# Performance work log

Measured on AMD Instinct MI355X. Metric: run time of the kernel, lower is better.

Reference implementation:

```python
import jax, jax.numpy as jnp
import numpy as np
import math

B, S, HID, L, NH, V, M = 8, 512, 768, 12, 12, 30522, 512
FF = 4 * HID
D = HID // NH


def sinusoidal_pe(seq_len, dim):
    pos = np.arange(seq_len, dtype=np.float32)[:, None]
    i = np.arange(dim // 2, dtype=np.float32)[None, :]
    ang = pos / np.power(10000.0, 2.0 * i / dim)
    pe = np.zeros((seq_len, dim), np.float32)
    pe[:, 0::2] = np.sin(ang)
    pe[:, 1::2] = np.cos(ang)
    return jnp.asarray(pe)


def setup_inputs() -> dict:
    key = jax.random.key(0)
    ks = iter(jax.random.split(key, 32))
    g = lambda sh: jax.random.normal(next(ks), sh, jnp.float32) * 0.02
    return {
        "token_ids": jax.random.randint(next(ks), (B, S), 0, V),
        "segment_info": jax.random.randint(next(ks), (B, S), 0, 2),
        "tok_emb": g((V, HID)),
        "seg_emb": g((3, HID)),
        "Wq": g((L, HID, HID)), "bq": jnp.zeros((L, HID)),
        "Wk": g((L, HID, HID)), "bk": jnp.zeros((L, HID)),
        "Wv": g((L, HID, HID)), "bv": jnp.zeros((L, HID)),
        "Wo": g((L, HID, HID)), "bo": jnp.zeros((L, HID)),
        "Wpk": g((L, HID, HID)),
        "Wpq": g((L, HID, HID)),
        "rel_emb": g((L, 2 * M, HID)),
        "ln1_g": jnp.ones((L, HID)), "ln1_b": jnp.zeros((L, HID)),
        "ln2_g": jnp.ones((L, HID)), "ln2_b": jnp.zeros((L, HID)),
        "W1": g((L, HID, FF)), "b1": jnp.zeros((L, FF)),
        "W2": g((L, FF, HID)), "b2": jnp.zeros((L, HID)),
        "lnf_g": jnp.ones((HID,)), "lnf_b": jnp.zeros((HID,)),
    }


def _ln(x, g, b):
    mu = x.mean(-1, keepdims=True)
    var = ((x - mu) ** 2).mean(-1, keepdims=True)
    return (x - mu) * jax.lax.rsqrt(var + 1e-5) * g + b


def _forward(token_ids, segment_info, tok_emb, seg_emb, layer_params, lnf_g, lnf_b):
    mask = token_ids != 0  # [B,S] valid-key mask
    x = tok_emb[token_ids] + sinusoidal_pe(S, HID)[None] + seg_emb[segment_info]
    qidx = jnp.arange(S)[:, None]
    # relative position bucket: clamp(q-k, -M, M-1) + M  -> [0, 2M)
    rel = jnp.clip(qidx - jnp.arange(S)[None, :], -M, M - 1) + M  # [S,S]
    scale = 1.0 / math.sqrt(3.0 * D)  # DeBERTa scales by sqrt(3d) for 3 score terms

    def body(x, p):
        (Wq, bq, Wk, bk, Wv, bv, Wo, bo, Wpk, Wpq, rel_e,
         l1g, l1b, l2g, l2b, W1, b1, W2, b2) = p
        # pre-norm attention sublayer
        h = _ln(x, l1g, l1b)
        q = (h @ Wq + bq).reshape(B, S, NH, D)
        k = (h @ Wk + bk).reshape(B, S, NH, D)
        v = (h @ Wv + bv).reshape(B, S, NH, D)
        c2c = jnp.einsum('bqhd,bkhd->bhqk', q, k)
        pk = (rel_e @ Wpk).reshape(2 * M, NH, D)
        pq = (rel_e @ Wpq).reshape(2 * M, NH, D)
        # content-to-position: Q_q . posK[rel(q,k)]
        c2p = jnp.einsum('bqhd,rhd->bhqr', q, pk)[:, :, qidx, rel]  # [B,NH,S,S]
        # position-to-content: K_k . posQ[rel(k,q)] -> gather over k rows then transpose
        p2c = jnp.einsum('bkhd,rhd->bhkr', k, pq)[:, :, qidx, rel]  # [B,NH,k,q]
        scores = (c2c + c2p + jnp.swapaxes(p2c, -1, -2)) * scale
        scores = jnp.where(mask[:, None, None, :], scores, -1e9)
        attn = jax.nn.softmax(scores, axis=-1)
        ctx = jnp.einsum('bhqk,bkhd->bqhd', attn, v).reshape(B, S, HID)
        x = x + ctx @ Wo + bo
        # pre-norm feedforward sublayer
        h2 = _ln(x, l2g, l2b)
        x = x + jax.nn.gelu(h2 @ W1 + b1, approximate=False) @ W2 + b2
        return x, None

    x, _ = jax.lax.scan(body, x, layer_params)
    return _ln(x, lnf_g, lnf_b)


def reference(token_ids, segment_info, tok_emb, seg_emb, Wq, bq, Wk, bk, Wv, bv,
              Wo, bo, Wpk, Wpq, rel_emb, ln1_g, ln1_b, ln2_g, ln2_b,
              W1, b1, W2, b2, lnf_g, lnf_b):
    lp = (Wq, bq, Wk, bk, Wv, bv, Wo, bo, Wpk, Wpq, rel_emb,
          ln1_g, ln1_b, ln2_g, ln2_b, W1, b1, W2, b2)
    return _forward(token_ids, segment_info, tok_emb, seg_emb, lp, lnf_g, lnf_b)
```

## Files before the change

### kernel.cpp

```cpp
#include <hip/hip_runtime.h>
#include <hip/hip_bf16.h>
#include <cstddef>
#include <cstdint>


constexpr int B   = 8;
constexpr int S   = 512;
constexpr int HID = 768;
constexpr int L   = 12;
constexpr int NH  = 12;
constexpr int D   = 64;
constexpr int FF  = 3072;
constexpr int M2  = 1024;
constexpr int NTOK = B * S;

using f32x4 = __attribute__((ext_vector_type(4))) float;
using s16x8 = __attribute__((ext_vector_type(8))) short;

__device__ inline float wave_sum(float v) {
#pragma unroll
  for (int o = 32; o > 0; o >>= 1) v += __shfl_xor(v, o, 64);
  return v;
}
__device__ inline unsigned short f2bf(float f) {
  __hip_bfloat16 h = __float2bfloat16(f);
  return *reinterpret_cast<unsigned short*>(&h);
}
__device__ inline float bf2f(unsigned short u) {
  union { unsigned int i; float f; } x;
  x.i = ((unsigned int)u) << 16;
  return x.f;
}
#define GLOAD16(gp, lp)                                                  \
  __builtin_amdgcn_global_load_lds(                                     \
      (const __attribute__((address_space(1))) void*)(gp),              \
      (__attribute__((address_space(3))) void*)(lp), 16, 0, 0)

__global__ void embed_kernel(const int* __restrict__ tok,
                             const int* __restrict__ seg,
                             const float* __restrict__ tok_emb,
                             const float* __restrict__ seg_emb,
                             float* __restrict__ x) {
  int row = blockIdx.x;
  int s = row & (S - 1);
  int t = tok[row];
  int sg = seg[row];
  for (int c = threadIdx.x; c < HID; c += blockDim.x) {
    int i = c >> 1;
    float ang = (float)s * powf(10000.0f, -2.0f * (float)i / (float)HID);
    float pe = (c & 1) ? cosf(ang) : sinf(ang);
    x[(size_t)row * HID + c] = tok_emb[(size_t)t * HID + c] + pe
                             + seg_emb[(size_t)sg * HID + c];
  }
}

template <int BF16OUT>
__global__ __launch_bounds__(256)
void ln_kernel(const float* __restrict__ in, void* __restrict__ outp,
               const float* __restrict__ g, const float* __restrict__ b,
               int nrows) {
  int wave = threadIdx.x >> 6, lane = threadIdx.x & 63;
  int row = blockIdx.x * 4 + wave;
  if (row >= nrows) return;
  const float* xr = in + (size_t)row * HID;
  float v[12];
  float s = 0.f;
#pragma unroll
  for (int i = 0; i < 12; i++) { v[i] = xr[lane + i * 64]; s += v[i]; }
  s = wave_sum(s);
  float mu = s * (1.0f / HID);
  float ss = 0.f;
#pragma unroll
  for (int i = 0; i < 12; i++) { float d = v[i] - mu; ss += d * d; }
  ss = wave_sum(ss);
  float inv = rsqrtf(ss * (1.0f / HID) + 1e-5f);
#pragma unroll
  for (int i = 0; i < 12; i++) {
    int c = lane + i * 64;
    float o = (v[i] - mu) * inv * g[c] + b[c];
    if (BF16OUT)
      ((unsigned short*)outp)[(size_t)row * HID + c] = f2bf(o);
    else
      ((float*)outp)[(size_t)row * HID + c] = o;
  }
}

__global__ __launch_bounds__(256)
void transpose6_kernel(const float* s0, const float* s1, const float* s2,
                       const float* s3, const float* s4, const float* s5,
                       unsigned short* __restrict__ dst) {
  const float* srcs[6] = {s0, s1, s2, s3, s4, s5};
  const float* src = srcs[blockIdx.z];
  unsigned short* d = dst + (size_t)blockIdx.z * HID * HID;
  __shared__ float tile[32][33];
  int nt = blockIdx.x * 32, kt = blockIdx.y * 32;
  int tx = threadIdx.x & 31, ty = threadIdx.x >> 5;
#pragma unroll
  for (int i = 0; i < 4; i++)
    tile[ty + i * 8][tx] = src[(size_t)(kt + ty + i * 8) * HID + nt + tx];
  __syncthreads();
#pragma unroll
  for (int i = 0; i < 4; i++)
    d[(size_t)(nt + ty + i * 8) * HID + kt + tx] = f2bf(tile[tx][ty + i * 8]);
}

__global__ __launch_bounds__(256)
void transpose_ff(const float* __restrict__ W1s, const float* __restrict__ W2s,
                  unsigned short* __restrict__ d1, unsigned short* __restrict__ d2) {
  const float* src = blockIdx.z ? W2s : W1s;
  unsigned short* dst = blockIdx.z ? d2 : d1;
  int K = blockIdx.z ? FF : HID;
  int N = blockIdx.z ? HID : FF;
  int nt, kt;
  if (blockIdx.z) { nt = blockIdx.y * 32; kt = blockIdx.x * 32; }
  else            { nt = blockIdx.x * 32; kt = blockIdx.y * 32; }
  __shared__ float tile[32][33];
  int tx = threadIdx.x & 31, ty = threadIdx.x >> 5;
#pragma unroll
  for (int i = 0; i < 4; i++)
    tile[ty + i * 8][tx] = src[(size_t)(kt + ty + i * 8) * N + nt + tx];
  __syncthreads();
#pragma unroll
  for (int i = 0; i < 4; i++)
    dst[(size_t)(nt + ty + i * 8) * K + kt + tx] = f2bf(tile[tx][ty + i * 8]);
}

__global__ void conv_bf16_kernel(const float* __restrict__ src,
                                 unsigned short* __restrict__ dst, int n) {
  int i = blockIdx.x * 256 + threadIdx.x;
  if (i < n) dst[i] = f2bf(src[i]);
}

__global__ void concat_bias(const float* __restrict__ bq,
                            const float* __restrict__ bk,
                            const float* __restrict__ bv,
                            float* __restrict__ bqkv) {
  int i = blockIdx.x * 256 + threadIdx.x;
  if (i >= L * 2304) return;
  int l = i / 2304, c = i % 2304;
  float v = (c < 768) ? bq[l * 768 + c]
          : (c < 1536) ? bk[l * 768 + c - 768] : bv[l * 768 + c - 1536];
  bqkv[i] = v;
}

template <int TN, int OUT_BF16, int GELU, int PARTIAL>
__global__ __launch_bounds__(256)
void mfma_gemm(const unsigned short* __restrict__ A,
               const unsigned short* __restrict__ Bt,
               const float* __restrict__ bias, const float* __restrict__ res,
               void* __restrict__ C, int Mr, int K, int N, int Kc) {
  constexpr int NW = TN / 32;
  __shared__ unsigned short As[128 * 32];
  __shared__ unsigned short Bs[TN * 32];
  int t = threadIdx.x, wave = t >> 6, lane = t & 63;
  int r0 = blockIdx.y * 128, n0 = blockIdx.x * TN;
  int kb = blockIdx.z * Kc;
  int wr = (wave >> 1) * 64;
  int wc = (wave & 1) * (TN / 2);

  f32x4 acc[4][NW] = {};
  int srow = lane >> 2, selem = (lane & 3) * 8;

  for (int k0 = kb; k0 < kb + Kc; k0 += 32) {
    __syncthreads();
    {
      const unsigned short* gA =
          A + (size_t)(r0 + wave * 32 + srow) * K + k0 + selem;
      unsigned short* lA = &As[(wave * 32) * 32];
      GLOAD16(gA, lA);
      GLOAD16(gA + (size_t)16 * K, lA + 16 * 32);
      if (TN == 128) {
        const unsigned short* gB =
            Bt + (size_t)(n0 + wave * 32 + srow) * K + k0 + selem;
        unsigned short* lB = &Bs[(wave * 32) * 32];
        GLOAD16(gB, lB);
        GLOAD16(gB + (size_t)16 * K, lB + 16 * 32);
      } else {
        const unsigned short* gB =
            Bt + (size_t)(n0 + wave * 16 + srow) * K + k0 + selem;
        GLOAD16(gB, &Bs[(wave * 16) * 32]);
      }
    }
    __syncthreads();

    s16x8 af[4], bf[NW];
#pragma unroll
    for (int m = 0; m < 4; m++)
      af[m] = *(const s16x8*)&As[(wr + m * 16 + (lane & 15)) * 32 + (lane >> 4) * 8];
#pragma unroll
    for (int n = 0; n < NW; n++)
      bf[n] = *(const s16x8*)&Bs[(wc + n * 16 + (lane & 15)) * 32 + (lane >> 4) * 8];
#pragma unroll
    for (int m = 0; m < 4; m++)
#pragma unroll
      for (int n = 0; n < NW; n++)
        acc[m][n] = __builtin_amdgcn_mfma_f32_16x16x32_bf16(af[m], bf[n],
                                                            acc[m][n], 0, 0, 0);
  }

  if (PARTIAL) {
    float* Cp = (float*)C + (size_t)blockIdx.z * Mr * N;
#pragma unroll
    for (int n = 0; n < NW; n++) {
      int c = n0 + wc + n * 16 + (lane & 15);
#pragma unroll
      for (int m = 0; m < 4; m++) {
        int rb = r0 + wr + m * 16 + ((lane >> 4) << 2);
#pragma unroll
        for (int j = 0; j < 4; j++)
          Cp[(size_t)(rb + j) * N + c] = acc[m][n][j];
      }
    }
    return;
  }
#pragma unroll
  for (int n = 0; n < NW; n++) {
    int c = n0 + wc + n * 16 + (lane & 15);
    float bv = bias ? bias[c] : 0.f;
#pragma unroll
    for (int m = 0; m < 4; m++) {
      int rb = r0 + wr + m * 16 + ((lane >> 4) << 2);
#pragma unroll
      for (int j = 0; j < 4; j++) {
        int r = rb + j;
        float val = acc[m][n][j] + bv;
        if (GELU) val = 0.5f * val * (1.0f + erff(val * 0.70710678118654752f));
        if (res)  val += res[(size_t)r * N + c];
        if (OUT_BF16)
          ((unsigned short*)C)[(size_t)r * N + c] = f2bf(val);
        else
          ((float*)C)[(size_t)r * N + c] = val;
      }
    }
  }
}

template <int LAST>
__global__ __launch_bounds__(256)
void combine_ln(const float* __restrict__ part,
                float* __restrict__ x, const float* __restrict__ bias,
                const float* __restrict__ g, const float* __restrict__ bb,
                void* __restrict__ outp) {
  int row = blockIdx.x, t = threadIdx.x;
  int wave = t >> 6, lane = t & 63;
  __shared__ float red[4];
  float v[3];
  float s = 0.f;
#pragma unroll
  for (int i = 0; i < 3; i++) {
    int c = t + i * 256;
    size_t idx = (size_t)row * HID + c;
    float val = x[idx] + part[idx] + part[(size_t)NTOK * HID + idx] + bias[c];
    if (!LAST) x[idx] = val;
    v[i] = val;
    s += val;
  }
  s = wave_sum(s);
  if (lane == 0) red[wave] = s;
  __syncthreads();
  float mu = (red[0] + red[1] + red[2] + red[3]) * (1.0f / HID);
  float ss = 0.f;
#pragma unroll
  for (int i = 0; i < 3; i++) { float d = v[i] - mu; ss += d * d; }
  ss = wave_sum(ss);
  __syncthreads();
  if (lane == 0) red[wave] = ss;
  __syncthreads();
  float inv = rsqrtf((red[0] + red[1] + red[2] + red[3]) * (1.0f / HID) + 1e-5f);
#pragma unroll
  for (int i = 0; i < 3; i++) {
    int c = t + i * 256;
    float o = (v[i] - mu) * inv * g[c] + bb[c];
    if (LAST)
      ((float*)outp)[(size_t)row * HID + c] = o;
    else
      ((unsigned short*)outp)[(size_t)row * HID + c] = f2bf(o);
  }
}

__global__ __launch_bounds__(256)
void transpose_v(const unsigned short* __restrict__ qkv,
                 unsigned short* __restrict__ vt) {
  __shared__ unsigned short tile[32][34];
  int bh = blockIdx.z;
  int b = bh / NH, h = bh % NH;
  int s0 = blockIdx.x * 32, d0 = blockIdx.y * 32;
  int tx = threadIdx.x & 31, ty = threadIdx.x >> 5;
#pragma unroll
  for (int i = 0; i < 4; i++)
    tile[ty + i * 8][tx] =
        qkv[(size_t)(b * S + s0 + ty + i * 8) * 2304 + 1536 + h * 64 + d0 + tx];
  __syncthreads();
#pragma unroll
  for (int i = 0; i < 4; i++)
    vt[((size_t)bh * 64 + d0 + ty + i * 8) * S + s0 + tx] = tile[tx][ty + i * 8];
}

__global__ __launch_bounds__(256)
void flash_attn(const unsigned short* __restrict__ qkv,
                const unsigned short* __restrict__ pkq,
                const unsigned short* __restrict__ vt,
                const int* __restrict__ tok,
                unsigned short* __restrict__ ctx) {
  constexpr int RS = 72, TS = 130;
  __shared__ unsigned short KPs[64 * RS];
  __shared__ unsigned short Vs[64 * RS];
  __shared__ unsigned short c2pL[64 * TS];
  __shared__ unsigned short p2cL[64 * TS];

  int t = threadIdx.x, wave = t >> 6, lane = t & 63;
  int bh = blockIdx.y;
  int b = bh / NH, h = bh % NH;
  int q0 = blockIdx.x * 64;
  int l15 = lane & 15, l4 = lane >> 4;
  const float scale = 0.07216878364870323f;

  s16x8 qf[2];
#pragma unroll
  for (int ks = 0; ks < 2; ks++)
    qf[ks] = *(const s16x8*)&qkv[(size_t)(b * S + q0 + wave * 16 + l15) * 2304
                                 + h * 64 + ks * 32 + l4 * 8];

  float m[4], l[4];
  f32x4 accO[4];
#pragma unroll
  for (int j = 0; j < 4; j++) { m[j] = -1e30f; l[j] = 0.f; }
#pragma unroll
  for (int n = 0; n < 4; n++) accO[n] = (f32x4){0.f, 0.f, 0.f, 0.f};

  for (int k0 = 0; k0 < S; k0 += 64) {
#pragma unroll
    for (int i = 0; i < 2; i++) {
      int c = t + i * 256;
      int r = c >> 3, d0 = (c & 7) * 8;
      *(s16x8*)&KPs[r * RS + d0] =
          *(const s16x8*)&qkv[(size_t)(b * S + k0 + r) * 2304 + 768 + h * 64 + d0];
      *(s16x8*)&Vs[r * RS + d0] =
          *(const s16x8*)&vt[((size_t)bh * 64 + r) * S + k0 + d0];
    }
    __syncthreads();

    int lo1 = q0 - k0 + 449;
    int lo2 = k0 - q0 + 449;
    f32x4 c2c[4] = {};
    f32x4 cp[8] = {}, pc[8] = {};
#pragma unroll
    for (int ks = 0; ks < 2; ks++) {
      int koff = ks * 32 + l4 * 8;
      s16x8 aq = qf[ks];
      s16x8 ak = *(const s16x8*)&KPs[(wave * 16 + l15) * RS + koff];
#pragma unroll
      for (int n = 0; n < 4; n++) {
        s16x8 bk = *(const s16x8*)&KPs[(n * 16 + l15) * RS + koff];
        c2c[n] = __builtin_amdgcn_mfma_f32_16x16x32_bf16(aq, bk, c2c[n], 0, 0, 0);
      }
#pragma unroll
      for (int tt = 0; tt < 8; tt++) {
        int rr = tt * 16 + l15;
        int r1 = lo1 + rr; r1 = r1 < 0 ? 0 : (r1 > M2 - 1 ? M2 - 1 : r1);
        int r2 = lo2 + rr; r2 = r2 < 0 ? 0 : (r2 > M2 - 1 ? M2 - 1 : r2);
        s16x8 bpk = *(const s16x8*)&pkq[(size_t)r1 * 1536 + h * 64 + koff];
        s16x8 bpq = *(const s16x8*)&pkq[(size_t)r2 * 1536 + 768 + h * 64 + koff];
        cp[tt] = __builtin_amdgcn_mfma_f32_16x16x32_bf16(aq, bpk, cp[tt], 0, 0, 0);
        pc[tt] = __builtin_amdgcn_mfma_f32_16x16x32_bf16(ak, bpq, pc[tt], 0, 0, 0);
      }
    }

    {
      int rw = wave * 16 + (l4 << 2);
#pragma unroll
      for (int tt = 0; tt < 8; tt++)
#pragma unroll
        for (int j = 0; j < 4; j++) {
          c2pL[(rw + j) * TS + tt * 16 + l15] = f2bf(cp[tt][j]);
          p2cL[(rw + j) * TS + tt * 16 + l15] = f2bf(pc[tt][j]);
        }
    }
    __syncthreads();

    float p[4][4];
    float rmax[4];
#pragma unroll
    for (int j = 0; j < 4; j++) rmax[j] = -1e30f;
#pragma unroll
    for (int n = 0; n < 4; n++) {
      int ik = n * 16 + l15;
      bool msk = (tok[b * S + k0 + ik] == 0);
#pragma unroll
      for (int j = 0; j < 4; j++) {
        int iq = wave * 16 + (l4 << 2) + j;
        float sc = c2c[n][j]
                 + bf2f(c2pL[iq * TS + (iq - ik + 63)])
                 + bf2f(p2cL[ik * TS + (ik - iq + 63)]);
        sc *= scale;
        if (msk) sc = -1e9f;
        p[n][j] = sc;
        rmax[j] = fmaxf(rmax[j], sc);
      }
    }
#pragma unroll
    for (int o = 8; o > 0; o >>= 1)
#pragma unroll
      for (int j = 0; j < 4; j++)
        rmax[j] = fmaxf(rmax[j], __shfl_xor(rmax[j], o, 64));
    float al[4];
#pragma unroll
    for (int j = 0; j < 4; j++) {
      float mn = fmaxf(m[j], rmax[j]);
      al[j] = __expf(m[j] - mn);
      m[j] = mn;
    }
    float rs[4] = {0.f, 0.f, 0.f, 0.f};
#pragma unroll
    for (int n = 0; n < 4; n++)
#pragma unroll
      for (int j = 0; j < 4; j++) {
        p[n][j] = __expf(p[n][j] - m[j]);
        rs[j] += p[n][j];
      }
#pragma unroll
    for (int o = 8; o > 0; o >>= 1)
#pragma unroll
      for (int j = 0; j < 4; j++) rs[j] += __shfl_xor(rs[j], o, 64);
#pragma unroll
    for (int j = 0; j < 4; j++) l[j] = l[j] * al[j] + rs[j];
#pragma unroll
    for (int n = 0; n < 4; n++)
#pragma unroll
      for (int j = 0; j < 4; j++) accO[n][j] *= al[j];

    {
      int rw = wave * 16 + (l4 << 2);
#pragma unroll
      for (int n = 0; n < 4; n++)
#pragma unroll
        for (int j = 0; j < 4; j++)
          KPs[(rw + j) * RS + n * 16 + l15] = f2bf(p[n][j]);
    }
    __syncthreads();

#pragma unroll
    for (int ks = 0; ks < 2; ks++) {
      int koff = ks * 32 + l4 * 8;
      s16x8 ap = *(const s16x8*)&KPs[(wave * 16 + l15) * RS + koff];
#pragma unroll
      for (int n = 0; n < 4; n++) {
        s16x8 bv2 = *(const s16x8*)&Vs[(n * 16 + l15) * RS + koff];
        accO[n] = __builtin_amdgcn_mfma_f32_16x16x32_bf16(ap, bv2, accO[n], 0, 0, 0);
      }
    }
    __syncthreads();
  }

#pragma unroll
  for (int n = 0; n < 4; n++) {
    int dd = h * 64 + n * 16 + l15;
#pragma unroll
    for (int j = 0; j < 4; j++) {
      int iq = q0 + wave * 16 + (l4 << 2) + j;
      ctx[(size_t)(b * S + iq) * HID + dd] = f2bf(accO[n][j] / l[j]);
    }
  }
}

extern "C" void kernel_launch(void* const* d_in, const int* in_sizes, int n_in,
                              void* d_out, int out_size, void* d_ws,
                              size_t ws_size, hipStream_t stream) {
  (void)in_sizes; (void)n_in; (void)out_size; (void)ws_size;
  const int*   tok     = (const int*)d_in[0];
  const int*   seg     = (const int*)d_in[1];
  const float* tok_emb = (const float*)d_in[2];
  const float* seg_emb = (const float*)d_in[3];
  const float* Wq  = (const float*)d_in[4];
  const float* bq  = (const float*)d_in[5];
  const float* Wk  = (const float*)d_in[6];
  const float* bk  = (const float*)d_in[7];
  const float* Wv  = (const float*)d_in[8];
  const float* bv  = (const float*)d_in[9];
  const float* Wo  = (const float*)d_in[10];
  const float* bo  = (const float*)d_in[11];
  const float* Wpk = (const float*)d_in[12];
  const float* Wpq = (const float*)d_in[13];
  const float* rel = (const float*)d_in[14];
  const float* ln1g = (const float*)d_in[15];
  const float* ln1b = (const float*)d_in[16];
  const float* ln2g = (const float*)d_in[17];
  const float* ln2b = (const float*)d_in[18];
  const float* W1  = (const float*)d_in[19];
  const float* b1  = (const float*)d_in[20];
  const float* W2  = (const float*)d_in[21];
  const float* b2  = (const float*)d_in[22];
  const float* lnfg = (const float*)d_in[23];
  const float* lnfb = (const float*)d_in[24];
  float* out = (float*)d_out;

  char* base = (char*)d_ws;
  size_t off = 0;
  auto alloc = [&](size_t bytes) -> void* {
    void* p = base + off;
    off += (bytes + 255) & ~(size_t)255;
    return p;
  };
  const size_t XSZ = (size_t)NTOK * HID;
  float* x = (float*)alloc(XSZ * 4);
  unsigned short* qkv16 = (unsigned short*)alloc((size_t)NTOK * 2304 * 2);
  unsigned short* pkq16 = (unsigned short*)alloc((size_t)M2 * 1536 * 2);
  unsigned short* vt16  = (unsigned short*)alloc(XSZ * 2);
  unsigned short* act16 = (unsigned short*)alloc(XSZ * 2);
  unsigned short* ff16  = (unsigned short*)alloc((size_t)NTOK * FF * 2);
  unsigned short* rel16 = (unsigned short*)alloc((size_t)M2 * HID * 2);
  unsigned short* wt6   = (unsigned short*)alloc((size_t)6 * HID * HID * 2);
  unsigned short* wt1   = (unsigned short*)alloc((size_t)HID * FF * 2);
  unsigned short* wt2   = (unsigned short*)alloc((size_t)HID * FF * 2);
  float* skbuf = (float*)alloc((size_t)2 * NTOK * HID * 4);
  float* bqkv  = (float*)alloc((size_t)L * 2304 * 4);

  const size_t WSQ = (size_t)HID * HID;

  embed_kernel<<<NTOK, 256, 0, stream>>>(tok, seg, tok_emb, seg_emb, x);
  concat_bias<<<(L * 2304 + 255) / 256, 256, 0, stream>>>(bq, bk, bv, bqkv);
  ln_kernel<1><<<NTOK / 4, 256, 0, stream>>>(x, act16, ln1g, ln1b, NTOK);

  for (int l = 0; l < L; l++) {
    transpose6_kernel<<<dim3(HID / 32, HID / 32, 6), 256, 0, stream>>>(
        Wq + l * WSQ, Wk + l * WSQ, Wv + l * WSQ, Wo + l * WSQ,
        Wpk + l * WSQ, Wpq + l * WSQ, wt6);
    transpose_ff<<<dim3(FF / 32, HID / 32, 2), 256, 0, stream>>>(
        W1 + (size_t)l * HID * FF, W2 + (size_t)l * FF * HID, wt1, wt2);
    conv_bf16_kernel<<<(M2 * HID + 255) / 256, 256, 0, stream>>>(
        rel + (size_t)l * M2 * HID, rel16, M2 * HID);

    mfma_gemm<128, 1, 0, 0><<<dim3(2304 / 128, NTOK / 128, 1), 256, 0, stream>>>(
        act16, wt6, bqkv + l * 2304, nullptr, qkv16, NTOK, HID, 2304, HID);
    mfma_gemm<64, 1, 0, 0><<<dim3(1536 / 64, M2 / 128, 1), 256, 0, stream>>>(
        rel16, wt6 + 4 * WSQ, nullptr, nullptr, pkq16, M2, HID, 1536, HID);
    transpose_v<<<dim3(S / 32, D / 32, B * NH), 256, 0, stream>>>(qkv16, vt16);
    flash_attn<<<dim3(S / 64, B * NH), 256, 0, stream>>>(
        qkv16, pkq16, vt16, tok, act16);
    mfma_gemm<64, 0, 0, 0><<<dim3(HID / 64, NTOK / 128, 1), 256, 0, stream>>>(
        act16, wt6 + 3 * WSQ, bo + l * HID, x, x, NTOK, HID, HID, HID);

    ln_kernel<1><<<NTOK / 4, 256, 0, stream>>>(x, act16, ln2g + l * HID,
                                               ln2b + l * HID, NTOK);
    mfma_gemm<128, 1, 1, 0><<<dim3(FF / 128, NTOK / 128, 1), 256, 0, stream>>>(
        act16, wt1, b1 + l * FF, nullptr, ff16, NTOK, HID, FF, HID);
    mfma_gemm<64, 0, 0, 1><<<dim3(HID / 64, NTOK / 128, 2), 256, 0, stream>>>(
        ff16, wt2, nullptr, nullptr, skbuf, NTOK, FF, HID, FF / 2);
    if (l < L - 1) {
      combine_ln<0><<<NTOK, 256, 0, stream>>>(
          skbuf, x, b2 + l * HID, ln1g + (l + 1) * HID, ln1b + (l + 1) * HID,
          act16);
    } else {
      combine_ln<1><<<NTOK, 256, 0, stream>>>(
          skbuf, x, b2 + l * HID, lnfg, lnfb, out);
    }
  }
}
```

Before: 4.694 ms.

## Stage relative-position band in LDS with XOR swizzle and merge weight prep kernels

Result: faster. 4.069 ms (-13.3%).

```diff
diff --git a/kernel.cpp b/kernel.cpp
--- a/kernel.cpp
+++ b/kernel.cpp
@@ -16,20 +16,24 @@
 
 using f32x4 = __attribute__((ext_vector_type(4))) float;
 using s16x8 = __attribute__((ext_vector_type(8))) short;
+typedef unsigned short us;
 
 __device__ inline float wave_sum(float v) {
 #pragma unroll
   for (int o = 32; o > 0; o >>= 1) v += __shfl_xor(v, o, 64);
   return v;
 }
-__device__ inline unsigned short f2bf(float f) {
+__device__ inline us f2bf(float f) {
   __hip_bfloat16 h = __float2bfloat16(f);
-  return *reinterpret_cast<unsigned short*>(&h);
-}
-__device__ inline float bf2f(unsigned short u) {
+  return *reinterpret_cast<us*>(&h);
+}
+__device__ inline float bf2f(us u) {
   union { unsigned int i; float f; } x;
   x.i = ((unsigned int)u) << 16;
   return x.f;
+}
+__device__ inline int swz8(int row, int g) {
+  return row * 64 + ((g ^ (row & 7)) << 3);
 }
 #define GLOAD16(gp, lp)                                                  \
   __builtin_amdgcn_global_load_lds(                                     \
@@ -79,43 +83,47 @@
     int c = lane + i * 64;
     float o = (v[i] - mu) * inv * g[c] + b[c];
     if (BF16OUT)
-      ((unsigned short*)outp)[(size_t)row * HID + c] = f2bf(o);
+      ((us*)outp)[(size_t)row * HID + c] = f2bf(o);
     else
       ((float*)outp)[(size_t)row * HID + c] = o;
   }
 }
 
 __global__ __launch_bounds__(256)
-void transpose6_kernel(const float* s0, const float* s1, const float* s2,
-                       const float* s3, const float* s4, const float* s5,
-                       unsigned short* __restrict__ dst) {
-  const float* srcs[6] = {s0, s1, s2, s3, s4, s5};
-  const float* src = srcs[blockIdx.z];
-  unsigned short* d = dst + (size_t)blockIdx.z * HID * HID;
-  __shared__ float tile[32][33];
-  int nt = blockIdx.x * 32, kt = blockIdx.y * 32;
-  int tx = threadIdx.x & 31, ty = threadIdx.x >> 5;
-#pragma unroll
-  for (int i = 0; i < 4; i++)
-    tile[ty + i * 8][tx] = src[(size_t)(kt + ty + i * 8) * HID + nt + tx];
-  __syncthreads();
-#pragma unroll
-  for (int i = 0; i < 4; i++)
-    d[(size_t)(nt + ty + i * 8) * HID + kt + tx] = f2bf(tile[tx][ty + i * 8]);
-}
-
-__global__ __launch_bounds__(256)
-void transpose_ff(const float* __restrict__ W1s, const float* __restrict__ W2s,
-                  unsigned short* __restrict__ d1, unsigned short* __restrict__ d2) {
-  const float* src = blockIdx.z ? W2s : W1s;
-  unsigned short* dst = blockIdx.z ? d2 : d1;
-  int K = blockIdx.z ? FF : HID;
-  int N = blockIdx.z ? HID : FF;
-  int nt, kt;
-  if (blockIdx.z) { nt = blockIdx.y * 32; kt = blockIdx.x * 32; }
-  else            { nt = blockIdx.x * 32; kt = blockIdx.y * 32; }
+void weight_prep(const float* Wq, const float* Wk, const float* Wv,
+                 const float* Wo, const float* Wpk, const float* Wpq,
+                 const float* W1s, const float* W2s, const float* rel,
+                 us* __restrict__ wt6, us* __restrict__ wt1,
+                 us* __restrict__ wt2, us* __restrict__ rel16) {
+  int bz = blockIdx.x;
+  if (bz >= 8064) {
+    int i = (bz - 8064) * 1024 + threadIdx.x * 4;
+    f32x4 v = *(const f32x4*)&rel[i];
+#pragma unroll
+    for (int j = 0; j < 4; j++) rel16[i + j] = f2bf(v[j]);
+    return;
+  }
   __shared__ float tile[32][33];
   int tx = threadIdx.x & 31, ty = threadIdx.x >> 5;
+  const float* src;
+  us* dst;
+  int N, K, nt, kt;
+  if (bz < 3456) {
+    int z = bz / 576, r = bz % 576;
+    const float* srcs[6] = {Wq, Wk, Wv, Wo, Wpk, Wpq};
+    src = srcs[z];
+    dst = wt6 + (size_t)z * HID * HID;
+    N = HID; K = HID;
+    nt = (r % 24) * 32; kt = (r / 24) * 32;
+  } else if (bz < 5760) {
+    int r = bz - 3456;
+    src = W1s; dst = wt1; N = FF; K = HID;
+    nt = (r % 96) * 32; kt = (r / 96) * 32;
+  } else {
+    int r = bz - 5760;
+    src = W2s; dst = wt2; N = HID; K = FF;
+    nt = (r % 24) * 32; kt = (r / 24) * 32;
+  }
 #pragma unroll
   for (int i = 0; i < 4; i++)
     tile[ty + i * 8][tx] = src[(size_t)(kt + ty + i * 8) * N + nt + tx];
@@ -123,12 +131,6 @@
 #pragma unroll
   for (int i = 0; i < 4; i++)
     dst[(size_t)(nt + ty + i * 8) * K + kt + tx] = f2bf(tile[tx][ty + i * 8]);
-}
-
-__global__ void conv_bf16_kernel(const float* __restrict__ src,
-                                 unsigned short* __restrict__ dst, int n) {
-  int i = blockIdx.x * 256 + threadIdx.x;
-  if (i < n) dst[i] = f2bf(src[i]);
 }
 
 __global__ void concat_bias(const float* __restrict__ bq,
@@ -145,13 +147,12 @@
 
 template <int TN, int OUT_BF16, int GELU, int PARTIAL>
 __global__ __launch_bounds__(256)
-void mfma_gemm(const unsigned short* __restrict__ A,
-               const unsigned short* __restrict__ Bt,
+void mfma_gemm(const us* __restrict__ A, const us* __restrict__ Bt,
                const float* __restrict__ bias, const float* __restrict__ res,
                void* __restrict__ C, int Mr, int K, int N, int Kc) {
   constexpr int NW = TN / 32;
-  __shared__ unsigned short As[128 * 32];
-  __shared__ unsigned short Bs[TN * 32];
+  __shared__ us As[128 * 32];
+  __shared__ us Bs[TN * 32];
   int t = threadIdx.x, wave = t >> 6, lane = t & 63;
   int r0 = blockIdx.y * 128, n0 = blockIdx.x * TN;
   int kb = blockIdx.z * Kc;
@@ -164,20 +165,17 @@
   for (int k0 = kb; k0 < kb + Kc; k0 += 32) {
     __syncthreads();
     {
-      const unsigned short* gA =
-          A + (size_t)(r0 + wave * 32 + srow) * K + k0 + selem;
-      unsigned short* lA = &As[(wave * 32) * 32];
+      const us* gA = A + (size_t)(r0 + wave * 32 + srow) * K + k0 + selem;
+      us* lA = &As[(wave * 32) * 32];
       GLOAD16(gA, lA);
       GLOAD16(gA + (size_t)16 * K, lA + 16 * 32);
       if (TN == 128) {
-        const unsigned short* gB =
-            Bt + (size_t)(n0 + wave * 32 + srow) * K + k0 + selem;
-        unsigned short* lB = &Bs[(wave * 32) * 32];
+        const us* gB = Bt + (size_t)(n0 + wave * 32 + srow) * K + k0 + selem;
+        us* lB = &Bs[(wave * 32) * 32];
         GLOAD16(gB, lB);
         GLOAD16(gB + (size_t)16 * K, lB + 16 * 32);
       } else {
-        const unsigned short* gB =
-            Bt + (size_t)(n0 + wave * 16 + srow) * K + k0 + selem;
+        const us* gB = Bt + (size_t)(n0 + wave * 16 + srow) * K + k0 + selem;
         GLOAD16(gB, &Bs[(wave * 16) * 32]);
       }
     }
@@ -227,7 +225,7 @@
         if (GELU) val = 0.5f * val * (1.0f + erff(val * 0.70710678118654752f));
         if (res)  val += res[(size_t)r * N + c];
         if (OUT_BF16)
-          ((unsigned short*)C)[(size_t)r * N + c] = f2bf(val);
+          ((us*)C)[(size_t)r * N + c] = f2bf(val);
         else
           ((float*)C)[(size_t)r * N + c] = val;
       }
@@ -274,14 +272,13 @@
     if (LAST)
       ((float*)outp)[(size_t)row * HID + c] = o;
     else
-      ((unsigned short*)outp)[(size_t)row * HID + c] = f2bf(o);
+      ((us*)outp)[(size_t)row * HID + c] = f2bf(o);
   }
 }
 
 __global__ __launch_bounds__(256)
-void transpose_v(const unsigned short* __restrict__ qkv,
-                 unsigned short* __restrict__ vt) {
-  __shared__ unsigned short tile[32][34];
+void transpose_v(const us* __restrict__ qkv, us* __restrict__ vt) {
+  __shared__ us tile[32][34];
   int bh = blockIdx.z;
   int b = bh / NH, h = bh % NH;
   int s0 = blockIdx.x * 32, d0 = blockIdx.y * 32;
@@ -296,17 +293,20 @@
     vt[((size_t)bh * 64 + d0 + ty + i * 8) * S + s0 + tx] = tile[tx][ty + i * 8];
 }
 
-__global__ __launch_bounds__(256)
-void flash_attn(const unsigned short* __restrict__ qkv,
-                const unsigned short* __restrict__ pkq,
-                const unsigned short* __restrict__ vt,
+__global__ __launch_bounds__(256, 3)
+void flash_attn(const us* __restrict__ qkv,
+                const us* __restrict__ pkq,
+                const us* __restrict__ vt,
                 const int* __restrict__ tok,
-                unsigned short* __restrict__ ctx) {
-  constexpr int RS = 72, TS = 130;
-  __shared__ unsigned short KPs[64 * RS];
-  __shared__ unsigned short Vs[64 * RS];
-  __shared__ unsigned short c2pL[64 * TS];
-  __shared__ unsigned short p2cL[64 * TS];
+                us* __restrict__ ctx) {
+  constexpr int TS = 130;
+  __shared__ us Ks[64 * 64];
+  __shared__ us Vs[64 * 64];
+  __shared__ us Band[16640];
+  us* PKb = Band;
+  us* PQb = Band + 8192;
+  us* c2pL = Band;
+  us* p2cL = Band + 8320;
 
   int t = threadIdx.x, wave = t >> 6, lane = t & 63;
   int bh = blockIdx.y;
@@ -332,39 +332,50 @@
 #pragma unroll
     for (int i = 0; i < 2; i++) {
       int c = t + i * 256;
-      int r = c >> 3, d0 = (c & 7) * 8;
-      *(s16x8*)&KPs[r * RS + d0] =
-          *(const s16x8*)&qkv[(size_t)(b * S + k0 + r) * 2304 + 768 + h * 64 + d0];
-      *(s16x8*)&Vs[r * RS + d0] =
-          *(const s16x8*)&vt[((size_t)bh * 64 + r) * S + k0 + d0];
-    }
-    __syncthreads();
-
+      int r = c >> 3, g = c & 7;
+      *(s16x8*)&Ks[swz8(r, g)] =
+          *(const s16x8*)&qkv[(size_t)(b * S + k0 + r) * 2304 + 768 + h * 64 + g * 8];
+      *(s16x8*)&Vs[swz8(r, g)] =
+          *(const s16x8*)&vt[((size_t)bh * 64 + r) * S + k0 + g * 8];
+    }
     int lo1 = q0 - k0 + 449;
     int lo2 = k0 - q0 + 449;
+#pragma unroll
+    for (int i = 0; i < 4; i++) {
+      int c = t + i * 256;
+      int r = c >> 3, g = c & 7;
+      int r1 = lo1 + r; r1 = r1 < 0 ? 0 : (r1 > M2 - 1 ? M2 - 1 : r1);
+      int r2 = lo2 + r; r2 = r2 < 0 ? 0 : (r2 > M2 - 1 ? M2 - 1 : r2);
+      *(s16x8*)&PKb[swz8(r, g)] =
+          *(const s16x8*)&pkq[(size_t)r1 * 1536 + h * 64 + g * 8];
+      *(s16x8*)&PQb[swz8(r, g)] =
+          *(const s16x8*)&pkq[(size_t)r2 * 1536 + 768 + h * 64 + g * 8];
+    }
+    __syncthreads();
+
     f32x4 c2c[4] = {};
     f32x4 cp[8] = {}, pc[8] = {};
 #pragma unroll
     for (int ks = 0; ks < 2; ks++) {
-      int koff = ks * 32 + l4 * 8;
-      s16x8 aq = qf[ks];
-      s16x8 ak = *(const s16x8*)&KPs[(wave * 16 + l15) * RS + koff];
+      int g = ks * 4 + l4;
+      int rA = wave * 16 + l15;
+      s16x8 ak = *(const s16x8*)&Ks[swz8(rA, g)];
 #pragma unroll
       for (int n = 0; n < 4; n++) {
-        s16x8 bk = *(const s16x8*)&KPs[(n * 16 + l15) * RS + koff];
-        c2c[n] = __builtin_amdgcn_mfma_f32_16x16x32_bf16(aq, bk, c2c[n], 0, 0, 0);
+        int rB = n * 16 + l15;
+        s16x8 bk = *(const s16x8*)&Ks[swz8(rB, g)];
+        c2c[n] = __builtin_amdgcn_mfma_f32_16x16x32_bf16(qf[ks], bk, c2c[n], 0, 0, 0);
       }
 #pragma unroll
       for (int tt = 0; tt < 8; tt++) {
         int rr = tt * 16 + l15;
-        int r1 = lo1 + rr; r1 = r1 < 0 ? 0 : (r1 > M2 - 1 ? M2 - 1 : r1);
-        int r2 = lo2 + rr; r2 = r2 < 0 ? 0 : (r2 > M2 - 1 ? M2 - 1 : r2);
-        s16x8 bpk = *(const s16x8*)&pkq[(size_t)r1 * 1536 + h * 64 + koff];
-        s16x8 bpq = *(const s16x8*)&pkq[(size_t)r2 * 1536 + 768 + h * 64 + koff];
-        cp[tt] = __builtin_amdgcn_mfma_f32_16x16x32_bf16(aq, bpk, cp[tt], 0, 0, 0);
+        s16x8 bpk = *(const s16x8*)&PKb[swz8(rr, g)];
+        s16x8 bpq = *(const s16x8*)&PQb[swz8(rr, g)];
+        cp[tt] = __builtin_amdgcn_mfma_f32_16x16x32_bf16(qf[ks], bpk, cp[tt], 0, 0, 0);
         pc[tt] = __builtin_amdgcn_mfma_f32_16x16x32_bf16(ak, bpq, pc[tt], 0, 0, 0);
       }
     }
+    __syncthreads();
 
     {
       int rw = wave * 16 + (l4 << 2);
@@ -434,18 +445,22 @@
 #pragma unroll
       for (int n = 0; n < 4; n++)
 #pragma unroll
-        for (int j = 0; j < 4; j++)
-          KPs[(rw + j) * RS + n * 16 + l15] = f2bf(p[n][j]);
+        for (int j = 0; j < 4; j++) {
+          int row = rw + j, col = n * 16 + l15;
+          Ks[row * 64 + (((col >> 3) ^ (row & 7)) << 3) + (col & 7)] = f2bf(p[n][j]);
+        }
     }
     __syncthreads();
 
 #pragma unroll
     for (int ks = 0; ks < 2; ks++) {
-      int koff = ks * 32 + l4 * 8;
-      s16x8 ap = *(const s16x8*)&KPs[(wave * 16 + l15) * RS + koff];
+      int g = ks * 4 + l4;
+      int rA = wave * 16 + l15;
+      s16x8 ap = *(const s16x8*)&Ks[swz8(rA, g)];
 #pragma unroll
       for (int n = 0; n < 4; n++) {
-        s16x8 bv2 = *(const s16x8*)&Vs[(n * 16 + l15) * RS + koff];
+        int rB = n * 16 + l15;
+        s16x8 bv2 = *(const s16x8*)&Vs[swz8(rB, g)];
         accO[n] = __builtin_amdgcn_mfma_f32_16x16x32_bf16(ap, bv2, accO[n], 0, 0, 0);
       }
     }
@@ -503,15 +518,15 @@
   };
   const size_t XSZ = (size_t)NTOK * HID;
   float* x = (float*)alloc(XSZ * 4);
-  unsigned short* qkv16 = (unsigned short*)alloc((size_t)NTOK * 2304 * 2);
-  unsigned short* pkq16 = (unsigned short*)alloc((size_t)M2 * 1536 * 2);
-  unsigned short* vt16  = (unsigned short*)alloc(XSZ * 2);
-  unsigned short* act16 = (unsigned short*)alloc(XSZ * 2);
-  unsigned short* ff16  = (unsigned short*)alloc((size_t)NTOK * FF * 2);
-  unsigned short* rel16 = (unsigned short*)alloc((size_t)M2 * HID * 2);
-  unsigned short* wt6   = (unsigned short*)alloc((size_t)6 * HID * HID * 2);
-  unsigned short* wt1   = (unsigned short*)alloc((size_t)HID * FF * 2);
-  unsigned short* wt2   = (unsigned short*)alloc((size_t)HID * FF * 2);
+  us* qkv16 = (us*)alloc((size_t)NTOK * 2304 * 2);
+  us* pkq16 = (us*)alloc((size_t)M2 * 1536 * 2);
+  us* vt16  = (us*)alloc(XSZ * 2);
+  us* act16 = (us*)alloc(XSZ * 2);
+  us* ff16  = (us*)alloc((size_t)NTOK * FF * 2);
+  us* rel16 = (us*)alloc((size_t)M2 * HID * 2);
+  us* wt6   = (us*)alloc((size_t)6 * HID * HID * 2);
+  us* wt1   = (us*)alloc((size_t)HID * FF * 2);
+  us* wt2   = (us*)alloc((size_t)HID * FF * 2);
   float* skbuf = (float*)alloc((size_t)2 * NTOK * HID * 4);
   float* bqkv  = (float*)alloc((size_t)L * 2304 * 4);
 
@@ -522,13 +537,11 @@
   ln_kernel<1><<<NTOK / 4, 256, 0, stream>>>(x, act16, ln1g, ln1b, NTOK);
 
   for (int l = 0; l < L; l++) {
-    transpose6_kernel<<<dim3(HID / 32, HID / 32, 6), 256, 0, stream>>>(
+    weight_prep<<<8832, 256, 0, stream>>>(
         Wq + l * WSQ, Wk + l * WSQ, Wv + l * WSQ, Wo + l * WSQ,
-        Wpk + l * WSQ, Wpq + l * WSQ, wt6);
-    transpose_ff<<<dim3(FF / 32, HID / 32, 2), 256, 0, stream>>>(
-        W1 + (size_t)l * HID * FF, W2 + (size_t)l * FF * HID, wt1, wt2);
-    conv_bf16_kernel<<<(M2 * HID + 255) / 256, 256, 0, stream>>>(
-        rel + (size_t)l * M2 * HID, rel16, M2 * HID);
+        Wpk + l * WSQ, Wpq + l * WSQ, W1 + (size_t)l * HID * FF,
+        W2 + (size_t)l * FF * HID, rel + (size_t)l * M2 * HID,
+        wt6, wt1, wt2, rel16);
 
     mfma_gemm<128, 1, 0, 0><<<dim3(2304 / 128, NTOK / 128, 1), 256, 0, stream>>>(
         act16, wt6, bqkv + l * 2304, nullptr, qkv16, NTOK, HID, 2304, HID);
```
